# Kernel tuning notes

Hardware: AMD Instinct MI355X
Metric: run time of the kernel (lower is better)

The kernel has to match this reference:

```python
import jax, jax.numpy as jnp
import numpy as np

N_NODES = 100000
N_EDGES = 300000
F_IN = 128
H = 256
L = 3


def setup_inputs() -> dict:
    key = jax.random.key(0)
    ks = jax.random.split(key, 8)
    s = 0.05
    return {
        "x": jax.random.normal(ks[0], (N_NODES, F_IN), dtype=jnp.float32),
        "edge_index": jax.random.randint(ks[1], (2, N_EDGES), 0, N_NODES, dtype=jnp.int32),
        "enc_w1": jax.random.normal(ks[2], (F_IN, H), dtype=jnp.float32) * s,
        "enc_b1": jnp.zeros((H,), dtype=jnp.float32),
        "enc_w2": jax.random.normal(ks[3], (H, H), dtype=jnp.float32) * s,
        "enc_b2": jnp.zeros((H,), dtype=jnp.float32),
        "gcn_w": jax.random.normal(ks[4], (L, H, H), dtype=jnp.float32) * s,
        "gcn_b": jnp.zeros((L, H), dtype=jnp.float32),
    }


def reference(x, edge_index, enc_w1, enc_b1, enc_w2, enc_b2, gcn_w, gcn_b):
    N = x.shape[0]
    # node_encoder: Linear -> ReLU -> (Dropout=id in eval) -> Linear
    h = jax.nn.relu(x @ enc_w1 + enc_b1) @ enc_w2 + enc_b2  # [N, H]

    # GCNConv normalization with self-loops (PyG default)
    loops = jnp.arange(N, dtype=edge_index.dtype)
    src = jnp.concatenate([edge_index[0], loops])  # [E+N]
    dst = jnp.concatenate([edge_index[1], loops])
    deg = jax.ops.segment_sum(jnp.ones_like(dst, dtype=h.dtype), dst, num_segments=N)
    dinv = jnp.where(deg > 0, jax.lax.rsqrt(deg), 0.0)
    norm = (dinv[src] * dinv[dst])[:, None]  # [E+N, 1]

    num_layers = gcn_w.shape[0]
    for l in range(num_layers):
        m = h @ gcn_w[l]  # transform [N, H]
        # gather messages from src, normalize, scatter-add to dst
        h = jax.ops.segment_sum(m[src] * norm, dst, num_segments=N) + gcn_b[l]
        h = jax.nn.relu(h)  # dropout is identity in eval mode
    return h
```

## Files before the change

kernel.cpp:

```cpp
#include <hip/hip_runtime.h>
#include <hip/hip_bf16.h>

#define NNODES 100000
#define NEDGES 300000
#define FIN 128
#define HDIM 256
#define NLAYERS 3
#define MPAD 100096

typedef float f32x4 __attribute__((ext_vector_type(4)));
typedef short bf16x8 __attribute__((ext_vector_type(8)));

__device__ inline float bf2f(unsigned short u) {
    union { unsigned int i; float f; } v;
    v.i = ((unsigned int)u) << 16;
    return v.f;
}
__device__ inline unsigned short f2bf(float f) {
    union { float f; unsigned int i; } v;
    v.f = f;
    return (unsigned short)((v.i + 0x7fffu + ((v.i >> 16) & 1u)) >> 16);
}

__device__ __forceinline__ void gll16(const unsigned short* g, unsigned short* l) {
    __builtin_amdgcn_global_load_lds(
        (const __attribute__((address_space(1))) unsigned int*)g,
        (__attribute__((address_space(3))) unsigned int*)l, 16, 0, 0);
}

template <int K, bool BIAS, bool RELU>
__global__ __launch_bounds__(256) void gemm_lds_k(
    const unsigned short* __restrict__ A, const unsigned short* __restrict__ Bt,
    const float* __restrict__ bias, unsigned short* __restrict__ C, int my) {
    constexpr int BK = 32;
    constexpr int NT = K / BK;
    __shared__ unsigned short sA[3][128 * BK];
    __shared__ unsigned short sB[3][128 * BK];

    const int bid   = blockIdx.x;
    const int ytile = (bid >> 4) * 8 + (bid & 7);
    if (ytile >= my) return;
    const int xcol  = (bid >> 3) & 1;
    const int rowblk = ytile * 128;
    const int colblk = xcol * 128;

    const int tid  = threadIdx.x;
    const int lane = tid & 63;
    const int wid  = tid >> 6;
    const int r15  = lane & 15;
    const int kq   = lane >> 4;
    const int wr   = wid >> 1;
    const int wc   = wid & 1;

    const unsigned short* gA[2];
    const unsigned short* gB[2];
    int ldsbase[2];
#pragma unroll
    for (int q = 0; q < 2; ++q) {
        int rr   = q * 64 + wid * 16 + (lane >> 2);
        int slot = (lane & 3) ^ ((rr >> 1) & 3);
        gA[q] = A  + (size_t)(rowblk + rr) * K + slot * 8;
        gB[q] = Bt + (size_t)(colblk + rr) * K + slot * 8;
        ldsbase[q] = (q * 64 + wid * 16) * BK;
    }

    const int sread = ((kq ^ ((r15 >> 1) & 3)) * 8);
    int aoff[4], boff[4];
#pragma unroll
    for (int i = 0; i < 4; ++i) {
        aoff[i] = (wr * 64 + i * 16 + r15) * BK + sread;
        boff[i] = (wc * 64 + i * 16 + r15) * BK + sread;
    }

    f32x4 acc[4][4] = {};

#pragma unroll
    for (int q = 0; q < 2; ++q) {
        gll16(gA[q], &sA[0][ldsbase[q]]);
        gll16(gB[q], &sB[0][ldsbase[q]]);
    }
#pragma unroll
    for (int q = 0; q < 2; ++q) {
        gll16(gA[q] + BK, &sA[1][ldsbase[q]]);
        gll16(gB[q] + BK, &sB[1][ldsbase[q]]);
    }

#pragma unroll
    for (int t = 0; t < NT; ++t) {
        if (t + 1 < NT) {
            asm volatile("s_waitcnt vmcnt(4)" ::: "memory");
        } else {
            asm volatile("s_waitcnt vmcnt(0)" ::: "memory");
        }
        __builtin_amdgcn_s_barrier();
        if (t + 2 < NT) {
#pragma unroll
            for (int q = 0; q < 2; ++q) {
                gll16(gA[q] + (t + 2) * BK, &sA[(t + 2) % 3][ldsbase[q]]);
                gll16(gB[q] + (t + 2) * BK, &sB[(t + 2) % 3][ldsbase[q]]);
            }
        }
        bf16x8 a[4], b[4];
#pragma unroll
        for (int i = 0; i < 4; ++i) a[i] = *(const bf16x8*)&sA[t % 3][aoff[i]];
#pragma unroll
        for (int j = 0; j < 4; ++j) b[j] = *(const bf16x8*)&sB[t % 3][boff[j]];
#pragma unroll
        for (int i = 0; i < 4; ++i)
#pragma unroll
            for (int j = 0; j < 4; ++j)
                acc[i][j] = __builtin_amdgcn_mfma_f32_16x16x32_bf16(a[i], b[j], acc[i][j], 0, 0, 0);
    }

#pragma unroll
    for (int i = 0; i < 4; ++i) {
#pragma unroll
        for (int reg = 0; reg < 4; ++reg) {
            int row = rowblk + wr * 64 + i * 16 + kq * 4 + reg;
#pragma unroll
            for (int j = 0; j < 4; ++j) {
                int col = colblk + wc * 64 + j * 16 + r15;
                float v = acc[i][j][reg];
                if (BIAS) v += bias[col];
                if (RELU) v = fmaxf(v, 0.0f);
                C[(size_t)row * HDIM + col] = f2bf(v);
            }
        }
    }
}

__global__ __launch_bounds__(256) void prep_k(
    const float* __restrict__ x, unsigned short* __restrict__ xb,
    const float* __restrict__ w1, unsigned short* __restrict__ w1t,
    const float* __restrict__ gw, unsigned short* __restrict__ gwt,
    const float* __restrict__ w2, unsigned short* __restrict__ w2c,
    const float* __restrict__ b2, float* __restrict__ foldb,
    unsigned* __restrict__ cnt) {
    int b = blockIdx.x;
    int tid = threadIdx.x;
    if (b < 12500) {
        int i = b * 256 + tid;
        float4 v = ((const float4*)x)[i];
        ushort4 u;
        u.x = f2bf(v.x); u.y = f2bf(v.y); u.z = f2bf(v.z); u.w = f2bf(v.w);
        ((ushort4*)xb)[i] = u;
    } else if (b < 12628) {
        int i = (b - 12500) * 256 + tid;
        int k = i >> 8, p = i & 255;
        w1t[(size_t)p * FIN + k] = f2bf(w1[i]);
    } else if (b < 13396) {
        int i = (b - 12628) * 256 + tid;
        int mat = i >> 16;
        int r = i & 65535;
        int k = r >> 8, p = r & 255;
        gwt[(size_t)mat * 65536 + (size_t)p * HDIM + k] = f2bf(gw[i]);
    } else if (b < 13460) {
        int i = (b - 13396) * 256 + tid;
        float4 v = ((const float4*)w2)[i];
        ushort4 u;
        u.x = f2bf(v.x); u.y = f2bf(v.y); u.z = f2bf(v.z); u.w = f2bf(v.w);
        ((ushort4*)w2c)[i] = u;
    } else if (b < 13851) {
        int i = (b - 13460) * 256 + tid;
        if (i < NNODES) cnt[i] = 0u;
    } else {
        int c = tid;
        float s = 0.0f;
#pragma unroll 8
        for (int j = 0; j < HDIM; ++j) s += b2[j] * gw[(size_t)j * HDIM + c];
        foldb[c] = s;
    }
}

__global__ void count_k(const int* __restrict__ dst, unsigned* __restrict__ cnt, int E) {
    int e = blockIdx.x * blockDim.x + threadIdx.x;
    if (e < E) atomicAdd(&cnt[dst[e]], 1u);
}

__global__ __launch_bounds__(256) void scan1_k(unsigned* __restrict__ cnt,
                                               int* __restrict__ rs,
                                               unsigned* __restrict__ blocksum,
                                               float* __restrict__ dinv, int N) {
    __shared__ unsigned tmp[256];
    int tid = threadIdx.x;
    int gid = blockIdx.x * 256 + tid;
    unsigned v = (gid < N) ? cnt[gid] : 0u;
    if (gid < N) {
        dinv[gid] = 1.0f / sqrtf((float)(v + 1u));
        cnt[gid] = 0u;
    }
    tmp[tid] = v;
    __syncthreads();
#pragma unroll
    for (int off = 1; off < 256; off <<= 1) {
        unsigned t = (tid >= off) ? tmp[tid - off] : 0u;
        __syncthreads();
        tmp[tid] += t;
        __syncthreads();
    }
    if (gid < N) rs[gid] = (int)(tmp[tid] - v);
    if (tid == 255) blocksum[blockIdx.x] = tmp[tid];
}

__global__ __launch_bounds__(512) void scan2_k(unsigned* __restrict__ blocksum, int nb) {
    __shared__ unsigned tmp[512];
    int tid = threadIdx.x;
    unsigned v = (tid < nb) ? blocksum[tid] : 0u;
    tmp[tid] = v;
    __syncthreads();
#pragma unroll
    for (int off = 1; off < 512; off <<= 1) {
        unsigned t = (tid >= off) ? tmp[tid - off] : 0u;
        __syncthreads();
        tmp[tid] += t;
        __syncthreads();
    }
    if (tid < nb) blocksum[tid] = tmp[tid] - v;
}

__global__ void scan3_k(int* __restrict__ rs, const unsigned* __restrict__ blocksum, int N, int E) {
    int gid = blockIdx.x * blockDim.x + threadIdx.x;
    if (gid < N) rs[gid] += (int)blocksum[gid >> 8];
    if (gid == 0) rs[N] = E;
}

__global__ void fill_k(const int* __restrict__ src, const int* __restrict__ dst,
                       const int* __restrict__ rs, unsigned* __restrict__ cursor,
                       const float* __restrict__ dinv,
                       int2* __restrict__ edata, int E) {
    int e = blockIdx.x * blockDim.x + threadIdx.x;
    if (e >= E) return;
    int s = src[e], d = dst[e];
    int pos = rs[d] + (int)atomicAdd(&cursor[d], 1u);
    float w = dinv[s] * dinv[d];
    edata[pos] = make_int2(s, __float_as_int(w));
}

template <bool OUTF32>
__global__ __launch_bounds__(256) void gather_k(const int* __restrict__ rs,
                                                const int2* __restrict__ edata,
                                                const float* __restrict__ dinv,
                                                const unsigned short* __restrict__ m,
                                                const float* __restrict__ bias,
                                                void* __restrict__ out, int N) {
    const int wid  = threadIdx.x >> 6;
    const int lane = threadIdx.x & 63;
    const int half = lane >> 5;
    const int hl   = lane & 31;
    const int node = blockIdx.x * 8 + wid * 2 + half;

    const int beg = rs[node], end = rs[node + 1];
    const float d = dinv[node];
    const float w0 = d * d;

    bf16x8 u = ((const bf16x8*)(m + (size_t)node * HDIM))[hl];
    float acc[8];
#pragma unroll
    for (int j = 0; j < 8; ++j) acc[j] = bf2f((unsigned short)u[j]) * w0;

    for (int base = beg; base < end; base += 32) {
        int2 ed = (base + hl < end) ? edata[base + hl] : make_int2(0, 0);
        int take = end - base;
        if (take > 32) take = 32;
        for (int e = 0; e < take; e += 4) {
            int s0 = __shfl(ed.x, half * 32 + e + 0);
            int s1 = __shfl(ed.x, half * 32 + e + 1);
            int s2 = __shfl(ed.x, half * 32 + e + 2);
            int s3 = __shfl(ed.x, half * 32 + e + 3);
            float wq0 = __int_as_float(__shfl(ed.y, half * 32 + e + 0));
            float wq1 = __int_as_float(__shfl(ed.y, half * 32 + e + 1));
            float wq2 = __int_as_float(__shfl(ed.y, half * 32 + e + 2));
            float wq3 = __int_as_float(__shfl(ed.y, half * 32 + e + 3));
            bf16x8 v0 = ((const bf16x8*)(m + (size_t)s0 * HDIM))[hl];
            bf16x8 v1 = ((const bf16x8*)(m + (size_t)s1 * HDIM))[hl];
            bf16x8 v2 = ((const bf16x8*)(m + (size_t)s2 * HDIM))[hl];
            bf16x8 v3 = ((const bf16x8*)(m + (size_t)s3 * HDIM))[hl];
#pragma unroll
            for (int j = 0; j < 8; ++j) {
                acc[j] += bf2f((unsigned short)v0[j]) * wq0;
                acc[j] += bf2f((unsigned short)v1[j]) * wq1;
                acc[j] += bf2f((unsigned short)v2[j]) * wq2;
                acc[j] += bf2f((unsigned short)v3[j]) * wq3;
            }
        }
    }

    float4 b0 = ((const float4*)bias)[hl * 2];
    float4 b1 = ((const float4*)bias)[hl * 2 + 1];
    acc[0] = fmaxf(acc[0] + b0.x, 0.0f); acc[1] = fmaxf(acc[1] + b0.y, 0.0f);
    acc[2] = fmaxf(acc[2] + b0.z, 0.0f); acc[3] = fmaxf(acc[3] + b0.w, 0.0f);
    acc[4] = fmaxf(acc[4] + b1.x, 0.0f); acc[5] = fmaxf(acc[5] + b1.y, 0.0f);
    acc[6] = fmaxf(acc[6] + b1.z, 0.0f); acc[7] = fmaxf(acc[7] + b1.w, 0.0f);

    if (OUTF32) {
        float4 o0 = {acc[0], acc[1], acc[2], acc[3]};
        float4 o1 = {acc[4], acc[5], acc[6], acc[7]};
        ((float4*)out)[(size_t)node * 64 + hl * 2] = o0;
        ((float4*)out)[(size_t)node * 64 + hl * 2 + 1] = o1;
    } else {
        bf16x8 o;
#pragma unroll
        for (int j = 0; j < 8; ++j) o[j] = (short)f2bf(acc[j]);
        ((bf16x8*)out)[(size_t)node * 32 + hl] = o;
    }
}

extern "C" void kernel_launch(void* const* d_in, const int* in_sizes, int n_in,
                              void* d_out, int out_size, void* d_ws, size_t ws_size,
                              hipStream_t stream) {
    const float* x  = (const float*)d_in[0];
    const int* ei   = (const int*)d_in[1];
    const float* w1 = (const float*)d_in[2];
    const float* b1 = (const float*)d_in[3];
    const float* w2 = (const float*)d_in[4];
    const float* b2 = (const float*)d_in[5];
    const float* gw = (const float*)d_in[6];
    const float* gb = (const float*)d_in[7];

    const int N = NNODES, E = NEDGES;
    const int* src = ei;
    const int* dst = ei + E;

    char* p = (char*)d_ws;
    unsigned short* h1   = (unsigned short*)p; p += (size_t)MPAD * HDIM * 2;
    unsigned short* h    = (unsigned short*)p; p += (size_t)MPAD * HDIM * 2;
    unsigned short* m    = (unsigned short*)p; p += (size_t)MPAD * HDIM * 2;
    unsigned short* w1t  = (unsigned short*)p; p += (size_t)FIN * HDIM * 2;
    unsigned short* gwt  = (unsigned short*)p; p += (size_t)NLAYERS * HDIM * HDIM * 2;
    unsigned short* w2c  = (unsigned short*)p; p += (size_t)HDIM * HDIM * 2;
    unsigned short* fBt  = (unsigned short*)p; p += (size_t)HDIM * HDIM * 2;
    float* foldb = (float*)p;          p += (size_t)HDIM * 4;
    unsigned* cnt = (unsigned*)p;      p += (size_t)N * 4;
    float* dinv = (float*)p;           p += (size_t)N * 4;
    int* rs = (int*)p;                 p += (size_t)(N + 1) * 4 + 12;
    unsigned* blocksum = (unsigned*)p; p += 512 * 4;
    int2* edata = (int2*)p;            p += (size_t)E * 8;

    unsigned short* xb = m;

    const int nb = (N + 255) / 256;
    const int MY = MPAD / 128;
    const int ggrid = 16 * ((MY + 7) / 8);

    prep_k<<<13852, 256, 0, stream>>>(x, xb, w1, w1t, gw, gwt, w2, w2c, b2, foldb, cnt);

    gemm_lds_k<HDIM, false, false><<<16, 256, 0, stream>>>(gwt, w2c, nullptr, fBt, 2);

    count_k<<<(E + 255) / 256, 256, 0, stream>>>(dst, cnt, E);
    scan1_k<<<nb, 256, 0, stream>>>(cnt, rs, blocksum, dinv, N);
    scan2_k<<<1, 512, 0, stream>>>(blocksum, nb);
    scan3_k<<<nb + 1, 256, 0, stream>>>(rs, blocksum, N, E);
    fill_k<<<(E + 255) / 256, 256, 0, stream>>>(src, dst, rs, cnt, dinv, edata, E);

    gemm_lds_k<FIN, true, true><<<ggrid, 256, 0, stream>>>(xb, w1t, b1, h1, MY);

    gemm_lds_k<HDIM, true, false><<<ggrid, 256, 0, stream>>>(h1, fBt, foldb, m, MY);
    gather_k<false><<<N / 8, 256, 0, stream>>>(rs, edata, dinv, m, gb, h, N);

    for (int l = 1; l < NLAYERS; ++l) {
        const unsigned short* wl = gwt + (size_t)l * HDIM * HDIM;
        const float* bl = gb + (size_t)l * HDIM;
        gemm_lds_k<HDIM, false, false><<<ggrid, 256, 0, stream>>>(h, wl, nullptr, m, MY);
        if (l < NLAYERS - 1)
            gather_k<false><<<N / 8, 256, 0, stream>>>(rs, edata, dinv, m, bl, h, N);
        else
            gather_k<true><<<N / 8, 256, 0, stream>>>(rs, edata, dinv, m, bl, d_out, N);
    }
}
```

Before: 421.6 us.

## Vectorize GEMM epilogue stores, fuse scan kernels, widen gather to 16 lanes per node

The GEMM swaps the MFMA operands so each lane holds four consecutive columns, which lets the epilogue write one ushort4 per fragment instead of scattered 2-byte stores. The two scan kernels become a single kernel in which each block sums the preceding block totals itself. The gather kernel now gives each node 16 lanes carrying 16 features each, so a wave handles four nodes and every lane issues twice as many independent row loads. The aim is fewer store transactions, one fewer launch, and more memory-level parallelism in the gather, at the cost of more registers per gather thread and some redundant prefix summing in the scan.

```diff
diff --git a/kernel.cpp b/kernel.cpp
--- a/kernel.cpp
+++ b/kernel.cpp
@@ -109,22 +109,27 @@
         for (int i = 0; i < 4; ++i)
 #pragma unroll
             for (int j = 0; j < 4; ++j)
-                acc[i][j] = __builtin_amdgcn_mfma_f32_16x16x32_bf16(a[i], b[j], acc[i][j], 0, 0, 0);
+                acc[i][j] = __builtin_amdgcn_mfma_f32_16x16x32_bf16(b[j], a[i], acc[i][j], 0, 0, 0);
     }
 
 #pragma unroll
     for (int i = 0; i < 4; ++i) {
-#pragma unroll
-        for (int reg = 0; reg < 4; ++reg) {
-            int row = rowblk + wr * 64 + i * 16 + kq * 4 + reg;
-#pragma unroll
-            for (int j = 0; j < 4; ++j) {
-                int col = colblk + wc * 64 + j * 16 + r15;
-                float v = acc[i][j][reg];
-                if (BIAS) v += bias[col];
-                if (RELU) v = fmaxf(v, 0.0f);
-                C[(size_t)row * HDIM + col] = f2bf(v);
+        int row = rowblk + wr * 64 + i * 16 + r15;
+#pragma unroll
+        for (int j = 0; j < 4; ++j) {
+            int colb = colblk + wc * 64 + j * 16 + kq * 4;
+            float v0 = acc[i][j][0], v1 = acc[i][j][1], v2 = acc[i][j][2], v3 = acc[i][j][3];
+            if (BIAS) {
+                float4 bb = ((const float4*)bias)[colb >> 2];
+                v0 += bb.x; v1 += bb.y; v2 += bb.z; v3 += bb.w;
             }
+            if (RELU) {
+                v0 = fmaxf(v0, 0.0f); v1 = fmaxf(v1, 0.0f);
+                v2 = fmaxf(v2, 0.0f); v3 = fmaxf(v3, 0.0f);
+            }
+            ushort4 o;
+            o.x = f2bf(v0); o.y = f2bf(v1); o.z = f2bf(v2); o.w = f2bf(v3);
+            *(ushort4*)&C[(size_t)row * HDIM + colb] = o;
         }
     }
 }
@@ -202,26 +207,21 @@
     if (tid == 255) blocksum[blockIdx.x] = tmp[tid];
 }
 
-__global__ __launch_bounds__(512) void scan2_k(unsigned* __restrict__ blocksum, int nb) {
-    __shared__ unsigned tmp[512];
-    int tid = threadIdx.x;
-    unsigned v = (tid < nb) ? blocksum[tid] : 0u;
-    tmp[tid] = v;
+__global__ __launch_bounds__(256) void scan23_k(int* __restrict__ rs,
+                                                const unsigned* __restrict__ blocksum,
+                                                int N, int E) {
+    const int b = blockIdx.x, tid = threadIdx.x;
+    unsigned s = 0;
+    for (int i = tid; i < b; i += 256) s += blocksum[i];
+    __shared__ unsigned red[4];
+#pragma unroll
+    for (int off = 32; off > 0; off >>= 1) s += __shfl_down(s, off);
+    if ((tid & 63) == 0) red[tid >> 6] = s;
     __syncthreads();
-#pragma unroll
-    for (int off = 1; off < 512; off <<= 1) {
-        unsigned t = (tid >= off) ? tmp[tid - off] : 0u;
-        __syncthreads();
-        tmp[tid] += t;
-        __syncthreads();
-    }
-    if (tid < nb) blocksum[tid] = tmp[tid] - v;
-}
-
-__global__ void scan3_k(int* __restrict__ rs, const unsigned* __restrict__ blocksum, int N, int E) {
-    int gid = blockIdx.x * blockDim.x + threadIdx.x;
-    if (gid < N) rs[gid] += (int)blocksum[gid >> 8];
-    if (gid == 0) rs[N] = E;
+    unsigned pref = red[0] + red[1] + red[2] + red[3];
+    int gid = b * 256 + tid;
+    if (gid < N) rs[gid] += (int)pref;
+    if (gid == N) rs[N] = E;
 }
 
 __global__ void fill_k(const int* __restrict__ src, const int* __restrict__ dst,
@@ -245,63 +245,82 @@
                                                 void* __restrict__ out, int N) {
     const int wid  = threadIdx.x >> 6;
     const int lane = threadIdx.x & 63;
-    const int half = lane >> 5;
-    const int hl   = lane & 31;
-    const int node = blockIdx.x * 8 + wid * 2 + half;
+    const int q    = lane >> 4;
+    const int ql   = lane & 15;
+    const int node = blockIdx.x * 16 + wid * 4 + q;
 
     const int beg = rs[node], end = rs[node + 1];
     const float d = dinv[node];
     const float w0 = d * d;
 
-    bf16x8 u = ((const bf16x8*)(m + (size_t)node * HDIM))[hl];
-    float acc[8];
-#pragma unroll
-    for (int j = 0; j < 8; ++j) acc[j] = bf2f((unsigned short)u[j]) * w0;
-
-    for (int base = beg; base < end; base += 32) {
-        int2 ed = (base + hl < end) ? edata[base + hl] : make_int2(0, 0);
+    const bf16x8* mrow = (const bf16x8*)(m + (size_t)node * HDIM);
+    bf16x8 u0 = mrow[ql * 2], u1 = mrow[ql * 2 + 1];
+    float acc[16];
+#pragma unroll
+    for (int j = 0; j < 8; ++j) {
+        acc[j]     = bf2f((unsigned short)u0[j]) * w0;
+        acc[8 + j] = bf2f((unsigned short)u1[j]) * w0;
+    }
+
+    for (int base = beg; base < end; base += 16) {
+        int2 ed = (base + ql < end) ? edata[base + ql] : make_int2(0, 0);
         int take = end - base;
-        if (take > 32) take = 32;
+        if (take > 16) take = 16;
         for (int e = 0; e < take; e += 4) {
-            int s0 = __shfl(ed.x, half * 32 + e + 0);
-            int s1 = __shfl(ed.x, half * 32 + e + 1);
-            int s2 = __shfl(ed.x, half * 32 + e + 2);
-            int s3 = __shfl(ed.x, half * 32 + e + 3);
-            float wq0 = __int_as_float(__shfl(ed.y, half * 32 + e + 0));
-            float wq1 = __int_as_float(__shfl(ed.y, half * 32 + e + 1));
-            float wq2 = __int_as_float(__shfl(ed.y, half * 32 + e + 2));
-            float wq3 = __int_as_float(__shfl(ed.y, half * 32 + e + 3));
-            bf16x8 v0 = ((const bf16x8*)(m + (size_t)s0 * HDIM))[hl];
-            bf16x8 v1 = ((const bf16x8*)(m + (size_t)s1 * HDIM))[hl];
-            bf16x8 v2 = ((const bf16x8*)(m + (size_t)s2 * HDIM))[hl];
-            bf16x8 v3 = ((const bf16x8*)(m + (size_t)s3 * HDIM))[hl];
+            int s0 = __shfl(ed.x, q * 16 + e + 0);
+            int s1 = __shfl(ed.x, q * 16 + e + 1);
+            int s2 = __shfl(ed.x, q * 16 + e + 2);
+            int s3 = __shfl(ed.x, q * 16 + e + 3);
+            float wq0 = __int_as_float(__shfl(ed.y, q * 16 + e + 0));
+            float wq1 = __int_as_float(__shfl(ed.y, q * 16 + e + 1));
+            float wq2 = __int_as_float(__shfl(ed.y, q * 16 + e + 2));
+            float wq3 = __int_as_float(__shfl(ed.y, q * 16 + e + 3));
+            const bf16x8* r0 = (const bf16x8*)(m + (size_t)s0 * HDIM);
+            const bf16x8* r1 = (const bf16x8*)(m + (size_t)s1 * HDIM);
+            const bf16x8* r2 = (const bf16x8*)(m + (size_t)s2 * HDIM);
+            const bf16x8* r3 = (const bf16x8*)(m + (size_t)s3 * HDIM);
+            bf16x8 v00 = r0[ql * 2], v01 = r0[ql * 2 + 1];
+            bf16x8 v10 = r1[ql * 2], v11 = r1[ql * 2 + 1];
+            bf16x8 v20 = r2[ql * 2], v21 = r2[ql * 2 + 1];
+            bf16x8 v30 = r3[ql * 2], v31 = r3[ql * 2 + 1];
 #pragma unroll
             for (int j = 0; j < 8; ++j) {
-                acc[j] += bf2f((unsigned short)v0[j]) * wq0;
-                acc[j] += bf2f((unsigned short)v1[j]) * wq1;
-                acc[j] += bf2f((unsigned short)v2[j]) * wq2;
-                acc[j] += bf2f((unsigned short)v3[j]) * wq3;
+                acc[j]     += bf2f((unsigned short)v00[j]) * wq0;
+                acc[8 + j] += bf2f((unsigned short)v01[j]) * wq0;
+                acc[j]     += bf2f((unsigned short)v10[j]) * wq1;
+                acc[8 + j] += bf2f((unsigned short)v11[j]) * wq1;
+                acc[j]     += bf2f((unsigned short)v20[j]) * wq2;
+                acc[8 + j] += bf2f((unsigned short)v21[j]) * wq2;
+                acc[j]     += bf2f((unsigned short)v30[j]) * wq3;
+                acc[8 + j] += bf2f((unsigned short)v31[j]) * wq3;
             }
         }
     }
 
-    float4 b0 = ((const float4*)bias)[hl * 2];
-    float4 b1 = ((const float4*)bias)[hl * 2 + 1];
-    acc[0] = fmaxf(acc[0] + b0.x, 0.0f); acc[1] = fmaxf(acc[1] + b0.y, 0.0f);
-    acc[2] = fmaxf(acc[2] + b0.z, 0.0f); acc[3] = fmaxf(acc[3] + b0.w, 0.0f);
-    acc[4] = fmaxf(acc[4] + b1.x, 0.0f); acc[5] = fmaxf(acc[5] + b1.y, 0.0f);
-    acc[6] = fmaxf(acc[6] + b1.z, 0.0f); acc[7] = fmaxf(acc[7] + b1.w, 0.0f);
+    float4 b0 = ((const float4*)bias)[ql * 4];
+    float4 b1 = ((const float4*)bias)[ql * 4 + 1];
+    float4 b2 = ((const float4*)bias)[ql * 4 + 2];
+    float4 b3 = ((const float4*)bias)[ql * 4 + 3];
+    float bb[16] = {b0.x, b0.y, b0.z, b0.w, b1.x, b1.y, b1.z, b1.w,
+                    b2.x, b2.y, b2.z, b2.w, b3.x, b3.y, b3.z, b3.w};
+#pragma unroll
+    for (int j = 0; j < 16; ++j) acc[j] = fmaxf(acc[j] + bb[j], 0.0f);
 
     if (OUTF32) {
-        float4 o0 = {acc[0], acc[1], acc[2], acc[3]};
-        float4 o1 = {acc[4], acc[5], acc[6], acc[7]};
-        ((float4*)out)[(size_t)node * 64 + hl * 2] = o0;
-        ((float4*)out)[(size_t)node * 64 + hl * 2 + 1] = o1;
+#pragma unroll
+        for (int k = 0; k < 4; ++k) {
+            float4 o = {acc[k * 4], acc[k * 4 + 1], acc[k * 4 + 2], acc[k * 4 + 3]};
+            ((float4*)out)[(size_t)node * 64 + ql * 4 + k] = o;
+        }
     } else {
-        bf16x8 o;
-#pragma unroll
-        for (int j = 0; j < 8; ++j) o[j] = (short)f2bf(acc[j]);
-        ((bf16x8*)out)[(size_t)node * 32 + hl] = o;
+        bf16x8 o0, o1;
+#pragma unroll
+        for (int j = 0; j < 8; ++j) {
+            o0[j] = (short)f2bf(acc[j]);
+            o1[j] = (short)f2bf(acc[8 + j]);
+        }
+        ((bf16x8*)out)[(size_t)node * 32 + ql * 2]     = o0;
+        ((bf16x8*)out)[(size_t)node * 32 + ql * 2 + 1] = o1;
     }
 }
 
@@ -348,22 +367,21 @@
 
     count_k<<<(E + 255) / 256, 256, 0, stream>>>(dst, cnt, E);
     scan1_k<<<nb, 256, 0, stream>>>(cnt, rs, blocksum, dinv, N);
-    scan2_k<<<1, 512, 0, stream>>>(blocksum, nb);
-    scan3_k<<<nb + 1, 256, 0, stream>>>(rs, blocksum, N, E);
+    scan23_k<<<nb, 256, 0, stream>>>(rs, blocksum, N, E);
     fill_k<<<(E + 255) / 256, 256, 0, stream>>>(src, dst, rs, cnt, dinv, edata, E);
 
     gemm_lds_k<FIN, true, true><<<ggrid, 256, 0, stream>>>(xb, w1t, b1, h1, MY);
 
     gemm_lds_k<HDIM, true, false><<<ggrid, 256, 0, stream>>>(h1, fBt, foldb, m, MY);
-    gather_k<false><<<N / 8, 256, 0, stream>>>(rs, edata, dinv, m, gb, h, N);
+    gather_k<false><<<N / 16, 256, 0, stream>>>(rs, edata, dinv, m, gb, h, N);
 
     for (int l = 1; l < NLAYERS; ++l) {
         const unsigned short* wl = gwt + (size_t)l * HDIM * HDIM;
         const float* bl = gb + (size_t)l * HDIM;
         gemm_lds_k<HDIM, false, false><<<ggrid, 256, 0, stream>>>(h, wl, nullptr, m, MY);
         if (l < NLAYERS - 1)
-            gather_k<false><<<N / 8, 256, 0, stream>>>(rs, edata, dinv, m, bl, h, N);
+            gather_k<false><<<N / 16, 256, 0, stream>>>(rs, edata, dinv, m, bl, h, N);
         else
-            gather_k<true><<<N / 8, 256, 0, stream>>>(rs, edata, dinv, m, bl, d_out, N);
-    }
-}
+            gather_k<true><<<N / 16, 256, 0, stream>>>(rs, edata, dinv, m, bl, d_out, N);
+    }
+}
```

Result: slower. 442.9 us (+5.1%).
